# Performance work log

Measured on AMD Instinct MI355X. Metric: run time of the kernel, lower is better.

## Reference

```python
import jax, jax.numpy as jnp
import numpy as np

N = 100_000   # nodes
E = 1_600_000 # edges (avg degree 16)
C = 64        # in/out channels
H = 64        # hidden width of pos_nn / attn_nn MLPs


def setup_inputs() -> dict:
    key = jax.random.key(0)
    ks = jax.random.split(key, 16)
    g = lambda k, s, fan: (jax.random.normal(k, s, jnp.float32) / np.float32(np.sqrt(fan)))
    return {
        "x": jax.random.normal(ks[0], (N, C), jnp.float32),
        "pos": jax.random.uniform(ks[1], (N, 2), jnp.float32),
        "edge_index": jax.random.randint(ks[2], (2, E), 0, N, jnp.int32),
        # linear_in (bias=True)
        "W_in": g(ks[3], (C, C), C), "b_in": jnp.zeros((C,), jnp.float32),
        # PointTransformerConv: lin (values), lin_src, lin_dst -- all bias=False in PyG
        "W_lin": g(ks[4], (C, C), C),
        "W_src": g(ks[5], (C, C), C),
        "W_dst": g(ks[6], (C, C), C),
        # pos_nn: MLP([2, 64, C], norm=None, plain_last=False) => Lin+ReLU, Lin+ReLU
        "Wp1": g(ks[7], (2, H), 2), "bp1": jnp.zeros((H,), jnp.float32),
        "Wp2": g(ks[8], (H, C), H), "bp2": jnp.zeros((C,), jnp.float32),
        # attn_nn: MLP([C, 64, C], norm=None, plain_last=False)
        "Wa1": g(ks[9], (C, H), C), "ba1": jnp.zeros((H,), jnp.float32),
        "Wa2": g(ks[10], (H, C), H), "ba2": jnp.zeros((C,), jnp.float32),
        # linear_out (bias=True)
        "W_out": g(ks[11], (C, C), C), "b_out": jnp.zeros((C,), jnp.float32),
    }


def reference(x, pos, edge_index, W_in, b_in, W_lin, W_src, W_dst,
              Wp1, bp1, Wp2, bp2, Wa1, ba1, Wa2, ba2, W_out, b_out):
    src = edge_index[0]  # j (message source)
    dst = edge_index[1]  # i (message target)

    # linear_in + relu
    h = jax.nn.relu(x @ W_in + b_in)                      # [N, C]

    # PointTransformerConv node projections
    a_dst = h @ W_dst                                     # alpha_i term [N, C]
    a_src = h @ W_src                                     # alpha_j term [N, C]
    v = h @ W_lin                                         # values     [N, C]

    # positional encoding delta = pos_nn(pos_i - pos_j)
    dpos = pos[dst] - pos[src]                            # [E, 2]
    delta = jax.nn.relu(jax.nn.relu(dpos @ Wp1 + bp1) @ Wp2 + bp2)  # [E, C]

    # attention logits: attn_nn(alpha_i - alpha_j + delta)
    a = a_dst[dst] - a_src[src] + delta                   # [E, C]
    a = jax.nn.relu(jax.nn.relu(a @ Wa1 + ba1) @ Wa2 + ba2)         # [E, C]

    # per-dst-node, per-channel segment softmax (PyG softmax with 1e-16 eps)
    amax = jax.ops.segment_max(a, dst, num_segments=N)    # [N, C]
    amax = jnp.where(jnp.isfinite(amax), amax, 0.0)
    ex = jnp.exp(a - amax[dst])                           # [E, C]
    denom = jax.ops.segment_sum(ex, dst, num_segments=N)  # [N, C]
    alpha = ex / (denom[dst] + 1e-16)                     # [E, C]

    # weighted scatter-aggregate of (v_j + delta)
    out = jax.ops.segment_sum(alpha * (v[src] + delta), dst, num_segments=N)  # [N, C]

    # linear_out + relu
    return jax.nn.relu(out @ W_out + b_out)
```

## Files before the change

kernel.cpp:

```cpp
#include <hip/hip_runtime.h>

#define N_NODES 100000
#define N_EDGES 1600000
#define NB (N_EDGES / 64)
#define PITCH 68
#define PITCHH 72
#define N_SCAN_BLOCKS ((N_NODES + 1023) / 1024)

typedef _Float16 half8 __attribute__((ext_vector_type(8)));
typedef float f32x4 __attribute__((ext_vector_type(4)));

__device__ __forceinline__ int wave_c0() {
  return __builtin_amdgcn_readfirstlane((int)((threadIdx.x >> 6) << 4));
}

template<bool RELU, bool BIAS>
__device__ __forceinline__ void wave_gemm16(const float* Alds, int lane, int c0,
                                            const float* __restrict__ W,
                                            const float* __restrict__ bias,
                                            float acc[16]) {
#pragma unroll
  for (int j = 0; j < 16; ++j) acc[j] = BIAS ? bias[c0 + j] : 0.0f;
  const float* arow = Alds + lane * PITCH;
#pragma unroll
  for (int k = 0; k < 64; k += 4) {
    const float4 a4 = *reinterpret_cast<const float4*>(arow + k);
    const float av[4] = {a4.x, a4.y, a4.z, a4.w};
#pragma unroll
    for (int kk = 0; kk < 4; ++kk) {
#pragma unroll
      for (int j = 0; j < 16; ++j)
        acc[j] = fmaf(av[kk], W[(k + kk) * 64 + c0 + j], acc[j]);
    }
  }
  if (RELU) {
#pragma unroll
    for (int j = 0; j < 16; ++j) acc[j] = fmaxf(acc[j], 0.0f);
  }
}

__device__ __forceinline__ void store4x4(float* dst, const float a[16]) {
#pragma unroll
  for (int q = 0; q < 4; ++q)
    *reinterpret_cast<float4*>(dst + q * 4) =
        make_float4(a[q * 4], a[q * 4 + 1], a[q * 4 + 2], a[q * 4 + 3]);
}

__device__ __forceinline__ void store16h(_Float16* dst, const float a[16]) {
  half8 h0, h1;
#pragma unroll
  for (int u = 0; u < 8; ++u) {
    h0[u] = (_Float16)a[u];
    h1[u] = (_Float16)a[8 + u];
  }
  *reinterpret_cast<half8*>(dst) = h0;
  *reinterpret_cast<half8*>(dst + 8) = h1;
}

__global__ __launch_bounds__(256) void wconv_kernel(const float* __restrict__ Wp2,
                                                    const float* __restrict__ Wa1,
                                                    const float* __restrict__ Wa2,
                                                    _Float16* __restrict__ wt) {
  int t = blockIdx.x * 256 + threadIdx.x;
  if (t >= 3 * 4096) return;
  int m = t >> 12, idx = t & 4095;
  int j = idx >> 6, k = idx & 63;
  const float* W = (m == 0) ? Wp2 : ((m == 1) ? Wa1 : Wa2);
  wt[m * 4096 + j * 64 + k] = (_Float16)W[k * 64 + j];
}

__global__ __launch_bounds__(256) void hist_kernel(const int* __restrict__ ei,
                                                   int* __restrict__ counts) {
  int e = blockIdx.x * 256 + threadIdx.x;
  if (e < N_EDGES) atomicAdd(&counts[ei[N_EDGES + e]], 1);
}

__global__ __launch_bounds__(1024) void scan1_kernel(const int* __restrict__ counts,
                                                     int* __restrict__ pexcl,
                                                     int* __restrict__ btot) {
  __shared__ int wsum[16];
  const int tid = threadIdx.x, lane = tid & 63, wid = tid >> 6;
  const int idx = blockIdx.x * 1024 + tid;
  const int val = (idx < N_NODES) ? counts[idx] : 0;
  int x = val;
#pragma unroll
  for (int o = 1; o < 64; o <<= 1) {
    int y = __shfl_up(x, o);
    if (lane >= o) x += y;
  }
  if (lane == 63) wsum[wid] = x;
  __syncthreads();
  if (wid == 0) {
    int s = (lane < 16) ? wsum[lane] : 0;
#pragma unroll
    for (int o = 1; o < 16; o <<= 1) {
      int y = __shfl_up(s, o);
      if (lane >= o) s += y;
    }
    if (lane < 16) wsum[lane] = s;
  }
  __syncthreads();
  const int woff = (wid > 0) ? wsum[wid - 1] : 0;
  const int incl = woff + x;
  if (idx < N_NODES) pexcl[idx] = incl - val;
  if (tid == 1023) btot[blockIdx.x] = incl;
}

__global__ __launch_bounds__(64) void scan2_kernel(int* __restrict__ btot) {
  const int lane = threadIdx.x;
  int carry = 0;
  for (int base = 0; base < N_SCAN_BLOCKS; base += 64) {
    const int ii = base + lane;
    const int v = (ii < N_SCAN_BLOCKS) ? btot[ii] : 0;
    int x = v;
#pragma unroll
    for (int o = 1; o < 64; o <<= 1) {
      int y = __shfl_up(x, o);
      if (lane >= o) x += y;
    }
    if (ii < N_SCAN_BLOCKS) btot[ii] = carry + x - v;
    carry += __shfl(x, 63);
  }
}

__global__ __launch_bounds__(256) void scan3_kernel(const int* __restrict__ pexcl,
                                                    const int* __restrict__ btot,
                                                    int* __restrict__ cursor) {
  const int idx = blockIdx.x * 256 + threadIdx.x;
  if (idx < N_NODES) cursor[idx] = pexcl[idx] + btot[idx >> 10];
}

__global__ __launch_bounds__(256) void scatter_kernel(const int* __restrict__ ei,
                                                      int* __restrict__ cursor,
                                                      int2* __restrict__ order2) {
  int e = blockIdx.x * 256 + threadIdx.x;
  if (e < N_EDGES) {
    int s = ei[e];
    int d = ei[N_EDGES + e];
    int p = atomicAdd(&cursor[d], 1);
    order2[p] = make_int2(s, d);
  }
}

__global__ __launch_bounds__(256) void node_proj_kernel(
    const float* __restrict__ x, const float* __restrict__ W_in,
    const float* __restrict__ b_in, const float* __restrict__ W_lin,
    const float* __restrict__ W_src, const float* __restrict__ W_dst,
    _Float16* __restrict__ adh, _Float16* __restrict__ ash,
    _Float16* __restrict__ vh) {
  __shared__ __align__(16) float A[64 * PITCH];
  const int tid = threadIdx.x, lane = tid & 63, c0 = wave_c0();
  const int n0 = blockIdx.x * 64;
#pragma unroll
  for (int i = 0; i < 4; ++i) {
    int idx4 = tid + i * 256;
    int e = idx4 >> 4, k4 = (idx4 & 15) * 4;
    int n = n0 + e;
    float4 val = make_float4(0.f, 0.f, 0.f, 0.f);
    if (n < N_NODES) val = *reinterpret_cast<const float4*>(x + (size_t)n * 64 + k4);
    *reinterpret_cast<float4*>(&A[e * PITCH + k4]) = val;
  }
  __syncthreads();
  float h[16];
  wave_gemm16<true, true>(A, lane, c0, W_in, b_in, h);
  __syncthreads();
  store4x4(&A[lane * PITCH + c0], h);
  __syncthreads();
  float o1[16], o2[16], o3[16];
  wave_gemm16<false, false>(A, lane, c0, W_dst, nullptr, o1);
  wave_gemm16<false, false>(A, lane, c0, W_src, nullptr, o2);
  wave_gemm16<false, false>(A, lane, c0, W_lin, nullptr, o3);
  const int n = n0 + lane;
  if (n < N_NODES) {
    store16h(adh + (size_t)n * 64 + c0, o1);
    store16h(ash + (size_t)n * 64 + c0, o2);
    store16h(vh + (size_t)n * 64 + c0, o3);
  }
}

__device__ __forceinline__ void mfma3(const _Float16* aL, int w, int g, int a,
                                      const _Float16* __restrict__ Wt,
                                      const float* __restrict__ bias,
                                      f32x4 acc[4]) {
  const half8 A0 = *reinterpret_cast<const half8*>(aL + (16 * w + a) * PITCHH + 8 * g);
  const half8 A1 = *reinterpret_cast<const half8*>(aL + (16 * w + a) * PITCHH + 32 + 8 * g);
#pragma unroll
  for (int t = 0; t < 4; ++t) {
    const half8 B0 = *reinterpret_cast<const half8*>(Wt + (16 * t + a) * 64 + 8 * g);
    const half8 B1 = *reinterpret_cast<const half8*>(Wt + (16 * t + a) * 64 + 32 + 8 * g);
    const float bv = bias[16 * t + a];
    f32x4 c = {bv, bv, bv, bv};
    c = __builtin_amdgcn_mfma_f32_16x16x32_f16(A0, B0, c, 0, 0, 0);
    c = __builtin_amdgcn_mfma_f32_16x16x32_f16(A1, B1, c, 0, 0, 0);
    acc[t] = c;
  }
}

__global__ __launch_bounds__(256) void edge_kernel(
    const int2* __restrict__ order2, const float* __restrict__ pos,
    const float* __restrict__ Wp1, const float* __restrict__ bp1,
    const _Float16* __restrict__ wt, const float* __restrict__ bp2,
    const float* __restrict__ ba1, const float* __restrict__ ba2,
    const _Float16* __restrict__ adh, const _Float16* __restrict__ ash,
    const _Float16* __restrict__ vh, float* __restrict__ num,
    float* __restrict__ den, float* __restrict__ pbuf,
    int* __restrict__ headd, int* __restrict__ taild) {
  __shared__ _Float16 s_act[64 * PITCHH];
  __shared__ _Float16 s_v[64 * PITCHH];
  const int tid = threadIdx.x, lane = tid & 63, w = tid >> 6;
  const int g = lane >> 4, a = lane & 15, c0 = w * 16;
  const int i = blockIdx.x * 64 + lane;
  const int2 sd = order2[i];
  const int d = sd.y;
  const int er = 16 * w + (lane >> 2);
  const int p = lane & 3;
  const int2 sd2 = order2[blockIdx.x * 64 + er];
  const int s2 = sd2.x, d2 = sd2.y;
  const _Float16* adr = adh + (size_t)d2 * 64 + 16 * p;
  const _Float16* asr = ash + (size_t)s2 * 64 + 16 * p;
  const _Float16* vr  = vh  + (size_t)s2 * 64 + 16 * p;
  const half8 ad0 = *reinterpret_cast<const half8*>(adr);
  const half8 ad1 = *reinterpret_cast<const half8*>(adr + 8);
  const half8 as0 = *reinterpret_cast<const half8*>(asr);
  const half8 as1 = *reinterpret_cast<const half8*>(asr + 8);
  const half8 v0  = *reinterpret_cast<const half8*>(vr);
  const half8 v1  = *reinterpret_cast<const half8*>(vr + 8);
  int dm1 = -1, dp1 = -1;
  if (lane == 0 && i > 0) dm1 = order2[i - 1].y;
  if (lane == 63 && i + 1 < N_EDGES) dp1 = order2[i + 1].y;
  dm1 = __shfl(dm1, 0);
  {
    const float2 pd = reinterpret_cast<const float2*>(pos)[d2];
    const float2 ps = reinterpret_cast<const float2*>(pos)[s2];
    const float dx = pd.x - ps.x, dy = pd.y - ps.y;
    half8 h0, h1;
#pragma unroll
    for (int u = 0; u < 8; ++u) {
      const int j0 = 16 * p + u, j1 = 16 * p + 8 + u;
      h0[u] = (_Float16)fmaxf(fmaf(dx, Wp1[j0], fmaf(dy, Wp1[64 + j0], bp1[j0])), 0.f);
      h1[u] = (_Float16)fmaxf(fmaf(dx, Wp1[j1], fmaf(dy, Wp1[64 + j1], bp1[j1])), 0.f);
    }
    *reinterpret_cast<half8*>(&s_act[er * PITCHH + 16 * p]) = h0;
    *reinterpret_cast<half8*>(&s_act[er * PITCHH + 16 * p + 8]) = h1;
  }
  f32x4 acc[4];
  mfma3(s_act, w, g, a, wt, bp2, acc);
#pragma unroll
  for (int t = 0; t < 4; ++t)
#pragma unroll
    for (int r = 0; r < 4; ++r)
      s_act[(16 * w + 4 * g + r) * PITCHH + 16 * t + a] =
          (_Float16)fmaxf(acc[t][r], 0.f);
  {
    const half8 dl0 = *reinterpret_cast<const half8*>(&s_act[er * PITCHH + 16 * p]);
    const half8 dl1 = *reinterpret_cast<const half8*>(&s_act[er * PITCHH + 16 * p + 8]);
    *reinterpret_cast<half8*>(&s_act[er * PITCHH + 16 * p]) = ad0 - as0 + dl0;
    *reinterpret_cast<half8*>(&s_act[er * PITCHH + 16 * p + 8]) = ad1 - as1 + dl1;
    *reinterpret_cast<half8*>(&s_v[er * PITCHH + 16 * p]) = v0 + dl0;
    *reinterpret_cast<half8*>(&s_v[er * PITCHH + 16 * p + 8]) = v1 + dl1;
  }
  mfma3(s_act, w, g, a, wt + 4096, ba1, acc);
#pragma unroll
  for (int t = 0; t < 4; ++t)
#pragma unroll
    for (int r = 0; r < 4; ++r)
      s_act[(16 * w + 4 * g + r) * PITCHH + 16 * t + a] =
          (_Float16)fmaxf(acc[t][r], 0.f);
  mfma3(s_act, w, g, a, wt + 2 * 4096, ba2, acc);
#pragma unroll
  for (int t = 0; t < 4; ++t)
#pragma unroll
    for (int r = 0; r < 4; ++r)
      s_act[(16 * w + 4 * g + r) * PITCHH + 16 * t + a] =
          (_Float16)__expf(fmaxf(acc[t][r], 0.f));
  __syncthreads();
  const half8 e0 = *reinterpret_cast<const half8*>(&s_act[lane * PITCHH + c0]);
  const half8 e1 = *reinterpret_cast<const half8*>(&s_act[lane * PITCHH + c0 + 8]);
  const half8 vd0 = *reinterpret_cast<const half8*>(&s_v[lane * PITCHH + c0]);
  const half8 vd1 = *reinterpret_cast<const half8*>(&s_v[lane * PITCHH + c0 + 8]);
  float vals[32];
#pragma unroll
  for (int j = 0; j < 16; ++j) {
    const float ex = (float)((j < 8) ? e0[j] : e1[j - 8]);
    const float vd = (float)((j < 8) ? vd0[j] : vd1[j - 8]);
    vals[j] = ex * vd;
    vals[16 + j] = ex;
  }
  const int dprev = __shfl_up(d, 1);
  const int dnext = __shfl_down(d, 1);
  const bool head = (lane == 0) || (d != dprev);
  const bool tail = (lane == 63) || (d != dnext);
  const unsigned long long hb = __ballot(head);
  const unsigned long long maskle =
      (lane == 63) ? ~0ull : ((1ull << (lane + 1)) - 1ull);
  const int myhead = 63 - __clzll(hb & maskle);
#pragma unroll
  for (int o = 1; o < 64; o <<= 1) {
    const bool c = (lane - o) >= myhead;
#pragma unroll
    for (int t = 0; t < 32; ++t) {
      float y = __shfl_up(vals[t], o);
      if (c) vals[t] += y;
    }
  }
  if (tail) {
    const bool ts = (myhead > 0) || (dm1 != d);
    const bool te = (lane < 63) || (dp1 != d);
    if (ts && te) {
      float* np = num + (size_t)d * 64 + c0;
      float* dp_ = den + (size_t)d * 64 + c0;
#pragma unroll
      for (int q = 0; q < 4; ++q)
        *reinterpret_cast<float4*>(np + 4 * q) =
            make_float4(vals[4 * q], vals[4 * q + 1], vals[4 * q + 2], vals[4 * q + 3]);
#pragma unroll
      for (int q = 0; q < 4; ++q)
        *reinterpret_cast<float4*>(dp_ + 4 * q) =
            make_float4(vals[16 + 4 * q], vals[17 + 4 * q], vals[18 + 4 * q],
                        vals[19 + 4 * q]);
    } else {
      const int slot = (!ts && te) ? 0 : 1;
      float* pb = pbuf + (size_t)blockIdx.x * 256 + slot * 128 + c0;
#pragma unroll
      for (int q = 0; q < 4; ++q)
        *reinterpret_cast<float4*>(pb + 4 * q) =
            make_float4(vals[4 * q], vals[4 * q + 1], vals[4 * q + 2], vals[4 * q + 3]);
#pragma unroll
      for (int q = 0; q < 4; ++q)
        *reinterpret_cast<float4*>(pb + 64 + 4 * q) =
            make_float4(vals[16 + 4 * q], vals[17 + 4 * q], vals[18 + 4 * q],
                        vals[19 + 4 * q]);
    }
    if (w == 0) {
      if (myhead == 0) headd[blockIdx.x] = ts ? -1 : (te ? d : -2);
      if (lane == 63) taild[blockIdx.x] = te ? -1 : d;
    }
  }
}

__global__ __launch_bounds__(128) void finish_kernel(
    const float* __restrict__ pbuf, const int* __restrict__ headd,
    const int* __restrict__ taild, float* __restrict__ num,
    float* __restrict__ den) {
  const int b = blockIdx.x + 1;
  const int t = taild[b - 1];
  if (t < 0) return;
  const int ch = threadIdx.x & 63, arr = threadIdx.x >> 6;
  const int h = headd[b];
  const float tv = pbuf[(size_t)(b - 1) * 256 + 128 + arr * 64 + ch];
  float* dst = (arr ? den : num) + (size_t)t * 64 + ch;
  if (h == t) {
    const float hv = pbuf[(size_t)b * 256 + arr * 64 + ch];
    if (headd[b - 1] != -2) {
      *dst = tv + hv;
    } else {
      atomicAdd(dst, tv + hv);
    }
  } else {
    atomicAdd(dst, tv);
  }
}

__global__ __launch_bounds__(256) void out_kernel(
    const float* __restrict__ num, const float* __restrict__ den,
    const float* __restrict__ W_out, const float* __restrict__ b_out,
    float* __restrict__ out) {
  __shared__ __align__(16) float A[64 * PITCH];
  const int tid = threadIdx.x, lane = tid & 63, c0 = wave_c0();
  const int n0 = blockIdx.x * 64;
#pragma unroll
  for (int i = 0; i < 4; ++i) {
    int idx4 = tid + i * 256;
    int e = idx4 >> 4, k4 = (idx4 & 15) * 4;
    int n = n0 + e;
    float4 val = make_float4(0.f, 0.f, 0.f, 0.f);
    if (n < N_NODES) {
      float4 nu = *reinterpret_cast<const float4*>(num + (size_t)n * 64 + k4);
      float4 de = *reinterpret_cast<const float4*>(den + (size_t)n * 64 + k4);
      val.x = nu.x / (de.x + 1e-16f);
      val.y = nu.y / (de.y + 1e-16f);
      val.z = nu.z / (de.z + 1e-16f);
      val.w = nu.w / (de.w + 1e-16f);
    }
    *reinterpret_cast<float4*>(&A[e * PITCH + k4]) = val;
  }
  __syncthreads();
  float o[16];
  wave_gemm16<true, true>(A, lane, c0, W_out, b_out, o);
  const int n = n0 + lane;
  if (n < N_NODES) store4x4(out + (size_t)n * 64 + c0, o);
}

extern "C" void kernel_launch(void* const* d_in, const int* in_sizes, int n_in,
                              void* d_out, int out_size, void* d_ws,
                              size_t ws_size, hipStream_t stream) {
  const float* x     = (const float*)d_in[0];
  const float* pos   = (const float*)d_in[1];
  const int*   ei    = (const int*)d_in[2];
  const float* W_in  = (const float*)d_in[3];
  const float* b_in  = (const float*)d_in[4];
  const float* W_lin = (const float*)d_in[5];
  const float* W_src = (const float*)d_in[6];
  const float* W_dst = (const float*)d_in[7];
  const float* Wp1   = (const float*)d_in[8];
  const float* bp1   = (const float*)d_in[9];
  const float* Wp2   = (const float*)d_in[10];
  const float* bp2   = (const float*)d_in[11];
  const float* Wa1   = (const float*)d_in[12];
  const float* ba1   = (const float*)d_in[13];
  const float* Wa2   = (const float*)d_in[14];
  const float* ba2   = (const float*)d_in[15];
  const float* W_out = (const float*)d_in[16];
  const float* b_out = (const float*)d_in[17];
  float* out = (float*)d_out;

  const size_t NC = (size_t)N_NODES * 64;
  _Float16* adh = (_Float16*)d_ws;
  _Float16* ash = adh + NC;
  _Float16* vh  = ash + NC;
  float* num = (float*)(vh + NC);
  float* den = num + NC;
  int* counts = (int*)(den + NC);
  int* cursor = counts + N_NODES;
  int* pexcl  = cursor + N_NODES;
  int* btot   = pexcl + N_NODES;
  int2* order2 = (int2*)(btot + 128);
  float* pbuf  = (float*)(order2 + N_EDGES);
  int* headd   = (int*)(pbuf + (size_t)NB * 256);
  int* taild   = headd + NB;
  _Float16* wt = (_Float16*)(taild + NB);

  hipMemsetAsync(num, 0, 2 * NC * sizeof(float), stream);
  hipMemsetAsync(counts, 0, N_NODES * sizeof(int), stream);

  wconv_kernel<<<48, 256, 0, stream>>>(Wp2, Wa1, Wa2, wt);
  hist_kernel<<<(N_EDGES + 255) / 256, 256, 0, stream>>>(ei, counts);
  scan1_kernel<<<N_SCAN_BLOCKS, 1024, 0, stream>>>(counts, pexcl, btot);
  scan2_kernel<<<1, 64, 0, stream>>>(btot);
  scan3_kernel<<<(N_NODES + 255) / 256, 256, 0, stream>>>(pexcl, btot, cursor);
  scatter_kernel<<<(N_EDGES + 255) / 256, 256, 0, stream>>>(ei, cursor, order2);

  node_proj_kernel<<<(N_NODES + 63) / 64, 256, 0, stream>>>(
      x, W_in, b_in, W_lin, W_src, W_dst, adh, ash, vh);
  edge_kernel<<<NB, 256, 0, stream>>>(
      order2, pos, Wp1, bp1, wt, bp2, ba1, ba2, adh, ash, vh, num, den,
      pbuf, headd, taild);
  finish_kernel<<<NB - 1, 128, 0, stream>>>(pbuf, headd, taild, num, den);
  out_kernel<<<(N_NODES + 63) / 64, 256, 0, stream>>>(num, den, W_out, b_out, out);
}
```

Before: 827.2 us.

## Replace wave shuffle segmented scan with MFMA segment-indicator matmul reduction

The per-destination segmented reduction of exp and exp*value, previously done with a 6-step shuffle scan over 32 registers per lane, is now done as a matrix product: a 0/1 segment-membership matrix in LDS is multiplied with transposed exp and exp*v tiles using f16 MFMA. Each segment's sums go straight to num/den or to the boundary buffer. This removes many cross-lane shuffles but adds LDS transposes, an extra LDS array and barrier, and computes exp*v products in fp16 rather than fp32.

```diff
diff --git a/kernel.cpp b/kernel.cpp
--- a/kernel.cpp
+++ b/kernel.cpp
@@ -205,11 +205,17 @@
     const _Float16* __restrict__ vh, float* __restrict__ num,
     float* __restrict__ den, float* __restrict__ pbuf,
     int* __restrict__ headd, int* __restrict__ taild) {
-  __shared__ _Float16 s_act[64 * PITCHH];
-  __shared__ _Float16 s_v[64 * PITCHH];
+  __shared__ __align__(16) _Float16 s_act[64 * PITCHH];
+  __shared__ __align__(16) _Float16 s_v[64 * PITCHH];
+  __shared__ __align__(16) _Float16 s_p[64 * PITCHH];
+  __shared__ int s_segd[64];
   const int tid = threadIdx.x, lane = tid & 63, w = tid >> 6;
   const int g = lane >> 4, a = lane & 15, c0 = w * 16;
   const int i = blockIdx.x * 64 + lane;
+#pragma unroll
+  for (int q = tid; q < 576; q += 256)
+    *reinterpret_cast<int4*>(&s_p[q * 8]) = make_int4(0, 0, 0, 0);
+  if (tid < 64) s_segd[tid] = -1;
   const int2 sd = order2[i];
   const int d = sd.y;
   const int er = 16 * w + (lane >> 2);
@@ -229,6 +235,15 @@
   if (lane == 0 && i > 0) dm1 = order2[i - 1].y;
   if (lane == 63 && i + 1 < N_EDGES) dp1 = order2[i + 1].y;
   dm1 = __shfl(dm1, 0);
+  dp1 = __shfl(dp1, 63);
+  const int dprev = __shfl_up(d, 1);
+  const bool head = (lane == 0) || (d != dprev);
+  const unsigned long long hb = __ballot(head);
+  const unsigned long long maskle =
+      (lane == 63) ? ~0ull : ((1ull << (lane + 1)) - 1ull);
+  const int sid = __popcll(hb & maskle) - 1;
+  const int nseg = __popcll(hb);
+  const int d0 = __shfl(d, 0), dl = __shfl(d, 63);
   {
     const float2 pd = reinterpret_cast<const float2*>(pos)[d2];
     const float2 ps = reinterpret_cast<const float2*>(pos)[s2];
@@ -278,62 +293,71 @@
   const half8 e1 = *reinterpret_cast<const half8*>(&s_act[lane * PITCHH + c0 + 8]);
   const half8 vd0 = *reinterpret_cast<const half8*>(&s_v[lane * PITCHH + c0]);
   const half8 vd1 = *reinterpret_cast<const half8*>(&s_v[lane * PITCHH + c0 + 8]);
-  float vals[32];
-#pragma unroll
-  for (int j = 0; j < 16; ++j) {
-    const float ex = (float)((j < 8) ? e0[j] : e1[j - 8]);
-    const float vd = (float)((j < 8) ? vd0[j] : vd1[j - 8]);
-    vals[j] = ex * vd;
-    vals[16 + j] = ex;
-  }
-  const int dprev = __shfl_up(d, 1);
-  const int dnext = __shfl_down(d, 1);
-  const bool head = (lane == 0) || (d != dprev);
-  const bool tail = (lane == 63) || (d != dnext);
-  const unsigned long long hb = __ballot(head);
-  const unsigned long long maskle =
-      (lane == 63) ? ~0ull : ((1ull << (lane + 1)) - 1ull);
-  const int myhead = 63 - __clzll(hb & maskle);
-#pragma unroll
-  for (int o = 1; o < 64; o <<= 1) {
-    const bool c = (lane - o) >= myhead;
-#pragma unroll
-    for (int t = 0; t < 32; ++t) {
-      float y = __shfl_up(vals[t], o);
-      if (c) vals[t] += y;
-    }
-  }
-  if (tail) {
-    const bool ts = (myhead > 0) || (dm1 != d);
-    const bool te = (lane < 63) || (dp1 != d);
-    if (ts && te) {
-      float* np = num + (size_t)d * 64 + c0;
-      float* dp_ = den + (size_t)d * 64 + c0;
-#pragma unroll
-      for (int q = 0; q < 4; ++q)
-        *reinterpret_cast<float4*>(np + 4 * q) =
-            make_float4(vals[4 * q], vals[4 * q + 1], vals[4 * q + 2], vals[4 * q + 3]);
-#pragma unroll
-      for (int q = 0; q < 4; ++q)
-        *reinterpret_cast<float4*>(dp_ + 4 * q) =
-            make_float4(vals[16 + 4 * q], vals[17 + 4 * q], vals[18 + 4 * q],
-                        vals[19 + 4 * q]);
-    } else {
-      const int slot = (!ts && te) ? 0 : 1;
-      float* pb = pbuf + (size_t)blockIdx.x * 256 + slot * 128 + c0;
-#pragma unroll
-      for (int q = 0; q < 4; ++q)
-        *reinterpret_cast<float4*>(pb + 4 * q) =
-            make_float4(vals[4 * q], vals[4 * q + 1], vals[4 * q + 2], vals[4 * q + 3]);
-#pragma unroll
-      for (int q = 0; q < 4; ++q)
-        *reinterpret_cast<float4*>(pb + 64 + 4 * q) =
-            make_float4(vals[16 + 4 * q], vals[17 + 4 * q], vals[18 + 4 * q],
-                        vals[19 + 4 * q]);
-    }
-    if (w == 0) {
-      if (myhead == 0) headd[blockIdx.x] = ts ? -1 : (te ? d : -2);
-      if (lane == 63) taild[blockIdx.x] = te ? -1 : d;
+  const half8 m0 = e0 * vd0;
+  const half8 m1 = e1 * vd1;
+  __syncthreads();
+#pragma unroll
+  for (int j = 0; j < 8; ++j) {
+    s_act[(c0 + j) * PITCHH + lane] = e0[j];
+    s_act[(c0 + 8 + j) * PITCHH + lane] = e1[j];
+    s_v[(c0 + j) * PITCHH + lane] = m0[j];
+    s_v[(c0 + 8 + j) * PITCHH + lane] = m1[j];
+  }
+  if (w == 0) {
+    s_p[sid * PITCHH + lane] = (_Float16)1.0f;
+    if (head) s_segd[sid] = d;
+  }
+  if (tid == 0) {
+    const bool ts0 = (dm1 != d0);
+    const bool te0 = (nseg > 1) || (dp1 != d0);
+    headd[blockIdx.x] = ts0 ? -1 : (te0 ? d0 : -2);
+    taild[blockIdx.x] = (dp1 != dl) ? -1 : dl;
+  }
+  __syncthreads();
+  if (16 * w < nseg) {
+    const half8 PA0 = *reinterpret_cast<const half8*>(&s_p[(16 * w + a) * PITCHH + 8 * g]);
+    const half8 PA1 = *reinterpret_cast<const half8*>(&s_p[(16 * w + a) * PITCHH + 32 + 8 * g]);
+    f32x4 accN[4], accD[4];
+#pragma unroll
+    for (int t = 0; t < 4; ++t) {
+      const half8 Bd0 = *reinterpret_cast<const half8*>(&s_act[(16 * t + a) * PITCHH + 8 * g]);
+      const half8 Bd1 = *reinterpret_cast<const half8*>(&s_act[(16 * t + a) * PITCHH + 32 + 8 * g]);
+      f32x4 cd = {0.f, 0.f, 0.f, 0.f};
+      cd = __builtin_amdgcn_mfma_f32_16x16x32_f16(PA0, Bd0, cd, 0, 0, 0);
+      cd = __builtin_amdgcn_mfma_f32_16x16x32_f16(PA1, Bd1, cd, 0, 0, 0);
+      accD[t] = cd;
+      const half8 Bn0 = *reinterpret_cast<const half8*>(&s_v[(16 * t + a) * PITCHH + 8 * g]);
+      const half8 Bn1 = *reinterpret_cast<const half8*>(&s_v[(16 * t + a) * PITCHH + 32 + 8 * g]);
+      f32x4 cn = {0.f, 0.f, 0.f, 0.f};
+      cn = __builtin_amdgcn_mfma_f32_16x16x32_f16(PA0, Bn0, cn, 0, 0, 0);
+      cn = __builtin_amdgcn_mfma_f32_16x16x32_f16(PA1, Bn1, cn, 0, 0, 0);
+      accN[t] = cn;
+    }
+#pragma unroll
+    for (int r = 0; r < 4; ++r) {
+      const int seg = 16 * w + 4 * g + r;
+      const int dseg = s_segd[seg];
+      if (dseg >= 0) {
+        const bool ts = (seg > 0) || (dm1 != dseg);
+        const bool te = (seg < nseg - 1) || (dp1 != dseg);
+        if (ts && te) {
+          float* np = num + (size_t)dseg * 64 + a;
+          float* dp_ = den + (size_t)dseg * 64 + a;
+#pragma unroll
+          for (int t = 0; t < 4; ++t) {
+            np[16 * t] = accN[t][r];
+            dp_[16 * t] = accD[t][r];
+          }
+        } else {
+          const int slot = (!ts && te) ? 0 : 1;
+          float* pb = pbuf + (size_t)blockIdx.x * 256 + slot * 128 + a;
+#pragma unroll
+          for (int t = 0; t < 4; ++t) {
+            pb[16 * t] = accN[t][r];
+            pb[64 + 16 * t] = accD[t][r];
+          }
+        }
+      }
     }
   }
 }
```

Result: faster. 788.3 us (-4.7%).
